# Kernel tuning notes

Hardware: AMD Instinct MI355X
Metric: run time of the kernel (lower is better)

The kernel has to match this reference:

```python
import jax, jax.numpy as jnp
import numpy as np

N_HEADS = 32
N_KV_HEADS = 8
DIM = 4096
HEAD_DIM = DIM // N_HEADS  # 128
N_REP = N_HEADS // N_KV_HEADS  # 4
MAX_B = 4
CACHE_LEN = 1024
SEQ = 1024
BATCH = 4


def _rope(t, cos, sin):
    # t: (b, s, h, hd); interpret last dim as interleaved complex pairs
    tr = t[..., 0::2]
    ti = t[..., 1::2]
    cos = cos[None, :, None, :]
    sin = sin[None, :, None, :]
    out_r = tr * cos - ti * sin
    out_i = tr * sin + ti * cos
    return jnp.stack([out_r, out_i], axis=-1).reshape(t.shape)


def setup_inputs() -> dict:
    key = jax.random.key(0)
    ks = jax.random.split(key, 6)
    x = jax.random.normal(ks[0], (BATCH, SEQ, DIM), dtype=jnp.float32)
    wq = jax.random.normal(ks[1], (DIM, N_HEADS * HEAD_DIM), dtype=jnp.float32) * (DIM ** -0.5)
    wk = jax.random.normal(ks[2], (DIM, N_KV_HEADS * HEAD_DIM), dtype=jnp.float32) * (DIM ** -0.5)
    wv = jax.random.normal(ks[3], (DIM, N_KV_HEADS * HEAD_DIM), dtype=jnp.float32) * (DIM ** -0.5)
    wo = jax.random.normal(ks[4], (DIM, DIM), dtype=jnp.float32) * (DIM ** -0.5)
    # standard RoPE frequencies, theta = 10000
    inv_freq = 1.0 / (10000.0 ** (np.arange(0, HEAD_DIM, 2, dtype=np.float32) / HEAD_DIM))
    pos = np.arange(SEQ, dtype=np.float32)
    ang = np.outer(pos, inv_freq)  # (SEQ, HEAD_DIM/2)
    freqs_cos = jnp.asarray(np.cos(ang), dtype=jnp.float32)
    freqs_sin = jnp.asarray(np.sin(ang), dtype=jnp.float32)
    return {"x": x, "freqs_cos": freqs_cos, "freqs_sin": freqs_sin,
            "wq": wq, "wk": wk, "wv": wv, "wo": wo, "start": 0}


def reference(x, freqs_cos, freqs_sin, wq, wk, wv, wo, start):
    b, s, _ = x.shape
    xq = (x @ wq).reshape(b, s, N_HEADS, HEAD_DIM)
    xk = (x @ wk).reshape(b, s, N_KV_HEADS, HEAD_DIM)
    xv = (x @ wv).reshape(b, s, N_KV_HEADS, HEAD_DIM)

    xq = _rope(xq, freqs_cos, freqs_sin)
    xk = _rope(xk, freqs_cos, freqs_sin)

    # KV cache append (cache initialized to zeros as in the module)
    cache_k = jnp.zeros((MAX_B, CACHE_LEN, N_KV_HEADS, HEAD_DIM), dtype=x.dtype)
    cache_v = jnp.zeros((MAX_B, CACHE_LEN, N_KV_HEADS, HEAD_DIM), dtype=x.dtype)
    cache_k = cache_k.at[:b, start:start + s].set(xk)
    cache_v = cache_v.at[:b, start:start + s].set(xv)

    keys = cache_k[:b, :start + s]    # (b, kv, n_kv, hd)
    values = cache_v[:b, :start + s]

    # repeat_kv to match query heads (GQA)
    keys = jnp.repeat(keys, N_REP, axis=2)      # (b, kv, n_q, hd)
    values = jnp.repeat(values, N_REP, axis=2)

    scale = 1.0 / jnp.sqrt(jnp.float32(HEAD_DIM)).astype(x.dtype)
    scores = jnp.einsum('bqhd,bkhd->bhqk', xq, keys) * scale
    probs = jax.nn.softmax(scores, axis=-1)
    out = jnp.einsum('bhqk,bkhd->bqhd', probs, values).reshape(b, s, DIM)
    return out @ wo
```

## Files before the change

kernel.cpp:

```cpp
#include <hip/hip_runtime.h>
#include <cstdint>

#define B_SZ 4
#define S_LEN 1024
#define DIM 4096
#define NH 32
#define KVH 8
#define HD 128
#define DQKV 6144

typedef __bf16 bf16x8 __attribute__((ext_vector_type(8)));
typedef float f32x4 __attribute__((ext_vector_type(4)));

__device__ __forceinline__ unsigned short f2bf(float f) {
  union { float f; uint32_t u; } v; v.f = f;
  uint32_t u = v.u;
  return (unsigned short)((u + 0x7fffu + ((u >> 16) & 1u)) >> 16);
}
__device__ __forceinline__ float bf2f(unsigned short h) {
  union { uint32_t u; float f; } v; v.u = ((uint32_t)h) << 16;
  return v.f;
}
__device__ __forceinline__ float ex2(float x) {
#if __has_builtin(__builtin_amdgcn_exp2f)
  return __builtin_amdgcn_exp2f(x);
#else
  return exp2f(x);
#endif
}

__device__ __forceinline__ void async16(void* lds, const void* g) {
  __builtin_amdgcn_global_load_lds(
      (const __attribute__((address_space(1))) void*)g,
      (__attribute__((address_space(3))) void*)lds, 16, 0, 0);
}

__global__ void cvt_x_kernel(const float* __restrict__ x, unsigned short* __restrict__ xb) {
  size_t i = ((size_t)blockIdx.x * 256 + threadIdx.x) * 4;
  float4 v = *(const float4*)(x + i);
  ushort4 o;
  o.x = f2bf(v.x); o.y = f2bf(v.y); o.z = f2bf(v.z); o.w = f2bf(v.w);
  *(ushort4*)(xb + i) = o;
}

__global__ void wtrans_kernel(const float* __restrict__ w, unsigned short* __restrict__ wt, int N) {
  __shared__ float tile[64][65];
  int n0 = blockIdx.x * 64, k0 = blockIdx.y * 64;
  int tx = threadIdx.x & 63, ty = threadIdx.x >> 6;
#pragma unroll
  for (int i = 0; i < 16; i++) {
    int k = ty + i * 4;
    tile[k][tx] = w[(size_t)(k0 + k) * N + n0 + tx];
  }
  __syncthreads();
  int c = threadIdx.x & 31, ny = threadIdx.x >> 5;
#pragma unroll
  for (int i = 0; i < 8; i++) {
    int n = ny + i * 8;
    ushort2 o;
    o.x = f2bf(tile[2 * c][n]);
    o.y = f2bf(tile[2 * c + 1][n]);
    *(ushort2*)(wt + (size_t)(n0 + n) * DIM + k0 + 2 * c) = o;
  }
}

template <bool OUT_BF16>
__global__ __launch_bounds__(512, 2) void gemm256_kernel(
    const unsigned short* __restrict__ A, const unsigned short* __restrict__ Bt,
    void* __restrict__ Cout, int Kdim, int ldc) {
  __shared__ __align__(16) unsigned short sh[3 * 16384];
  const int tid = threadIdx.x;
  const int wave = tid >> 6, lane = tid & 63;
  const int nbx = gridDim.x;
  const int nb = nbx * (int)gridDim.y;
  const int bid = (int)blockIdx.y * nbx + (int)blockIdx.x;
  const int sb = (bid & 7) * (nb >> 3) + (bid >> 3);
  const int m0 = (sb / nbx) * 256, n0 = (sb % nbx) * 256;

  const int r0 = tid >> 2;
  const int cs = (tid & 3) ^ ((r0 >> 1) & 3);
  const unsigned short* gA = A + (size_t)(m0 + r0) * Kdim + cs * 8;
  const unsigned short* gB = Bt + (size_t)(n0 + r0) * Kdim + cs * 8;
  const size_t halfstep = (size_t)128 * Kdim;

  const int wm = wave >> 2, wn = wave & 3;
  const int rl = lane & 15, lh4 = lane >> 4;
  const int pcl = lh4 ^ ((rl >> 1) & 3);
  const int aoff = (wm * 128 + rl) * 32 + pcl * 8;
  const int boff = (wn * 64 + rl) * 32 + pcl * 8;

  f32x4 acc[8][4] = {};

#define STAGE(CB, KO) do {                                        \
    unsigned short* dst = sh + (CB) * 16384 + wave * 512;         \
    async16(dst,          gA + (KO));                             \
    async16(dst + 4096,   gA + halfstep + (KO));                  \
    async16(dst + 8192,   gB + (KO));                             \
    async16(dst + 12288,  gB + halfstep + (KO));                  \
  } while (0)

#define COMPUTE(CB) do {                                                          \
    const unsigned short* bufA = sh + (CB) * 16384;                               \
    const unsigned short* bufB = bufA + 8192;                                     \
    bf16x8 bfr[4], afr[4];                                                        \
    _Pragma("unroll") for (int n = 0; n < 4; n++)                                 \
      bfr[n] = *(const bf16x8*)(bufB + boff + n * 512);                           \
    _Pragma("unroll") for (int m = 0; m < 4; m++)                                 \
      afr[m] = *(const bf16x8*)(bufA + aoff + m * 512);                           \
    __builtin_amdgcn_s_setprio(1);                                                \
    _Pragma("unroll") for (int m = 0; m < 4; m++)                                 \
      _Pragma("unroll") for (int n = 0; n < 4; n++)                               \
        acc[m][n] = __builtin_amdgcn_mfma_f32_16x16x32_bf16(afr[m], bfr[n], acc[m][n], 0, 0, 0); \
    __builtin_amdgcn_s_setprio(0);                                                \
    asm volatile("s_barrier" ::: "memory");                                       \
    _Pragma("unroll") for (int m = 0; m < 4; m++)                                 \
      afr[m] = *(const bf16x8*)(bufA + aoff + (m + 4) * 512);                     \
    __builtin_amdgcn_s_setprio(1);                                                \
    _Pragma("unroll") for (int m = 0; m < 4; m++)                                 \
      _Pragma("unroll") for (int n = 0; n < 4; n++)                               \
        acc[m + 4][n] = __builtin_amdgcn_mfma_f32_16x16x32_bf16(afr[m], bfr[n], acc[m + 4][n], 0, 0, 0); \
    __builtin_amdgcn_s_setprio(0);                                                \
  } while (0)

  STAGE(0, 0);
  STAGE(1, 32);
  STAGE(2, 64);
  const int NT = Kdim >> 5;
  int cb = 0;
  for (int t = 0; t < NT - 3; ++t) {
    asm volatile("s_waitcnt vmcnt(8)" ::: "memory");
    asm volatile("s_barrier" ::: "memory");
    COMPUTE(cb);
    asm volatile("s_waitcnt lgkmcnt(0)" ::: "memory");
    asm volatile("s_barrier" ::: "memory");
    STAGE(cb, (size_t)(t + 3) * 32);
    cb = cb == 2 ? 0 : cb + 1;
  }
  asm volatile("s_waitcnt vmcnt(8)" ::: "memory");
  asm volatile("s_barrier" ::: "memory");
  COMPUTE(cb);
  cb = cb == 2 ? 0 : cb + 1;
  asm volatile("s_waitcnt vmcnt(4)" ::: "memory");
  asm volatile("s_barrier" ::: "memory");
  COMPUTE(cb);
  cb = cb == 2 ? 0 : cb + 1;
  asm volatile("s_waitcnt vmcnt(0)" ::: "memory");
  asm volatile("s_barrier" ::: "memory");
  COMPUTE(cb);
#undef STAGE
#undef COMPUTE

#pragma unroll
  for (int m = 0; m < 8; m++)
#pragma unroll
    for (int n = 0; n < 4; n++)
#pragma unroll
      for (int reg = 0; reg < 4; reg++) {
        int row = m0 + wm * 128 + m * 16 + lh4 * 4 + reg;
        int col = n0 + wn * 64 + n * 16 + rl;
        float v = acc[m][n][reg];
        if (OUT_BF16)
          ((unsigned short*)Cout)[(size_t)row * ldc + col] = f2bf(v);
        else
          ((float*)Cout)[(size_t)row * ldc + col] = v;
      }
}

__global__ void rope_kernel(const unsigned short* __restrict__ src, const float* __restrict__ fc,
                            const float* __restrict__ fs, unsigned short* __restrict__ dst,
                            int nheads, int hshift, float scale) {
  int idx = blockIdx.x * 256 + threadIdx.x;
  int f4 = idx & 15;
  int rest = idx >> 4;
  int hh = rest & (nheads - 1);
  int t = rest >> hshift;
  int s = t & (S_LEN - 1);
  int b = t >> 10;
  union { uint4 v; unsigned short u[8]; } in, out;
  in.v = *(const uint4*)(src + (size_t)t * DQKV + hh * HD + f4 * 8);
  union { float4 v; float f[4]; } c4, s4;
  c4.v = *(const float4*)(fc + s * 64 + f4 * 4);
  s4.v = *(const float4*)(fs + s * 64 + f4 * 4);
#pragma unroll
  for (int j = 0; j < 4; j++) {
    float xr = bf2f(in.u[2 * j]), xi = bf2f(in.u[2 * j + 1]);
    float cc = c4.f[j], ss = s4.f[j];
    out.u[2 * j] = f2bf((xr * cc - xi * ss) * scale);
    out.u[2 * j + 1] = f2bf((xr * ss + xi * cc) * scale);
  }
  *(uint4*)(dst + ((size_t)(b * nheads + hh) * S_LEN + s) * HD + f4 * 8) = out.v;
}

__global__ void vtrans_kernel(const unsigned short* __restrict__ src, unsigned short* __restrict__ Vt) {
  __shared__ __align__(16) unsigned short tile[32][33];
  int s0 = blockIdx.x * 32, d0 = blockIdx.y * 32, bk = blockIdx.z;
  int tx = threadIdx.x & 31, ty = threadIdx.x >> 5;
#pragma unroll
  for (int i = 0; i < 4; i++) {
    int s = ty + i * 8;
    tile[s][tx] = src[(size_t)((bk >> 3) * S_LEN + s0 + s) * DQKV + (bk & 7) * HD + d0 + tx];
  }
  __syncthreads();
#pragma unroll
  for (int i = 0; i < 4; i++) {
    int d = ty + i * 8;
    Vt[((size_t)bk * HD + d0 + d) * S_LEN + s0 + tx] = tile[tx][d];
  }
}

__global__ __launch_bounds__(256, 3) void attn_kernel(
    const unsigned short* __restrict__ Qb,
    const unsigned short* __restrict__ Kb,
    const unsigned short* __restrict__ Vt,
    unsigned short* __restrict__ Ob) {
  __shared__ __align__(16) unsigned short Kt[64][128];
  __shared__ __align__(16) unsigned short Vl[128][64];
  __shared__ __align__(16) unsigned short Pl[4][16][72];
  const int tid = threadIdx.x, wave = tid >> 6, lane = tid & 63;
  const int qb = blockIdx.x, h = blockIdx.y, b = blockIdx.z;
  const int kvh = h >> 2;
  const int lql = lane & 15, lqh = lane >> 4;
  const int qrow = qb * 64 + wave * 16;

  const unsigned short* Qp = Qb + ((size_t)(b * NH + h) * S_LEN + qrow + lql) * HD + lqh * 8;
  bf16x8 qf[4];
#pragma unroll
  for (int kd = 0; kd < 4; kd++) qf[kd] = *(const bf16x8*)(Qp + kd * 32);

  const unsigned short* Kp = Kb + (size_t)(b * KVH + kvh) * S_LEN * HD;
  const unsigned short* Vp = Vt + (size_t)(b * KVH + kvh) * HD * S_LEN;
  const int krow_in = lane >> 4;
  const int kcol_sw = lane & 15;
  const int vrow_in = lane >> 3;
  const int vcol_off = ((lane & 7) ^ (lane >> 3)) * 8;

  float m_run[4], l_run[4];
  f32x4 Oacc[8] = {};
#pragma unroll
  for (int r = 0; r < 4; r++) { m_run[r] = -3.0e38f; l_run[r] = 0.0f; }

  for (int kt = 0; kt < S_LEN; kt += 64) {
    __syncthreads();
#pragma unroll
    for (int j = 0; j < 4; j++) {
      int rbase = wave * 16 + j * 4;
      int r = rbase + krow_in;
      async16(&Kt[rbase][0], Kp + (size_t)(kt + r) * HD + ((kcol_sw ^ (r & 7)) * 8));
    }
#pragma unroll
    for (int j = 0; j < 4; j++) {
      int dbase = wave * 32 + j * 8;
      int d = dbase + vrow_in;
      async16(&Vl[dbase][0], Vp + (size_t)d * S_LEN + kt + vcol_off);
    }
    __syncthreads();
    f32x4 sf[4] = {};
#pragma unroll
    for (int ni = 0; ni < 4; ni++) {
      const int ksw = lql & 7;
#pragma unroll
      for (int kd = 0; kd < 4; kd++) {
        bf16x8 kf = *(const bf16x8*)(&Kt[ni * 16 + lql][((kd * 4 + lqh) ^ ksw) * 8]);
        sf[ni] = __builtin_amdgcn_mfma_f32_16x16x32_bf16(qf[kd], kf, sf[ni], 0, 0, 0);
      }
    }
    float mnew[4], alpha[4], psum[4];
#pragma unroll
    for (int r = 0; r < 4; r++) {
      float v = fmaxf(fmaxf(sf[0][r], sf[1][r]), fmaxf(sf[2][r], sf[3][r]));
      v = fmaxf(v, __shfl_xor(v, 1));
      v = fmaxf(v, __shfl_xor(v, 2));
      v = fmaxf(v, __shfl_xor(v, 4));
      v = fmaxf(v, __shfl_xor(v, 8));
      mnew[r] = fmaxf(m_run[r], v);
      alpha[r] = ex2(m_run[r] - mnew[r]);
      m_run[r] = mnew[r];
      psum[r] = 0.0f;
    }
#pragma unroll
    for (int ni = 0; ni < 4; ni++)
#pragma unroll
      for (int r = 0; r < 4; r++) {
        float p = ex2(sf[ni][r] - mnew[r]);
        psum[r] += p;
        union { float f; uint32_t u; } pv; pv.f = p;
        Pl[wave][lqh * 4 + r][ni * 16 + lql] = (unsigned short)(pv.u >> 16);
      }
#pragma unroll
    for (int r = 0; r < 4; r++) {
      float v = psum[r];
      v += __shfl_xor(v, 1);
      v += __shfl_xor(v, 2);
      v += __shfl_xor(v, 4);
      v += __shfl_xor(v, 8);
      l_run[r] = l_run[r] * alpha[r] + v;
    }
#pragma unroll
    for (int ni = 0; ni < 8; ni++)
#pragma unroll
      for (int r = 0; r < 4; r++) Oacc[ni][r] *= alpha[r];
    bf16x8 pa[2];
#pragma unroll
    for (int ks = 0; ks < 2; ks++)
      pa[ks] = *(const bf16x8*)(&Pl[wave][lql][ks * 32 + lqh * 8]);
#pragma unroll
    for (int ni = 0; ni < 8; ni++) {
      const int ksw = lql & 7;
#pragma unroll
      for (int ks = 0; ks < 2; ks++) {
        bf16x8 vb = *(const bf16x8*)(&Vl[ni * 16 + lql][((ks * 4 + lqh) ^ ksw) * 8]);
        Oacc[ni] = __builtin_amdgcn_mfma_f32_16x16x32_bf16(pa[ks], vb, Oacc[ni], 0, 0, 0);
      }
    }
  }
#pragma unroll
  for (int r = 0; r < 4; r++) l_run[r] = 1.0f / l_run[r];
#pragma unroll
  for (int ni = 0; ni < 8; ni++)
#pragma unroll
    for (int r = 0; r < 4; r++) {
      int q = qrow + lqh * 4 + r;
      Ob[(size_t)(b * S_LEN + q) * DIM + h * HD + ni * 16 + lql] = f2bf(Oacc[ni][r] * l_run[r]);
    }
}

extern "C" void kernel_launch(void* const* d_in, const int* in_sizes, int n_in,
                              void* d_out, int out_size, void* d_ws, size_t ws_size,
                              hipStream_t stream) {
  (void)in_sizes; (void)n_in; (void)out_size; (void)ws_size;
  const float* x  = (const float*)d_in[0];
  const float* fc = (const float*)d_in[1];
  const float* fs = (const float*)d_in[2];
  const float* wq = (const float*)d_in[3];
  const float* wk = (const float*)d_in[4];
  const float* wv = (const float*)d_in[5];
  const float* wo = (const float*)d_in[6];
  float* out = (float*)d_out;
  char* ws = (char*)d_ws;

  const size_t MB = 1024 * 1024;
  unsigned short* xb    = (unsigned short*)(ws + 0);
  unsigned short* attnb = (unsigned short*)(ws + 0);
  unsigned short* wqkvt = (unsigned short*)(ws + 32 * MB);
  unsigned short* Qb    = (unsigned short*)(ws + 32 * MB);
  unsigned short* Kb    = (unsigned short*)(ws + 64 * MB);
  unsigned short* Vt    = (unsigned short*)(ws + 72 * MB);
  unsigned short* wot   = (unsigned short*)(ws + 80 * MB);
  unsigned short* qkv   = (unsigned short*)(ws + 112 * MB);

  cvt_x_kernel<<<16384, 256, 0, stream>>>(x, xb);
  wtrans_kernel<<<dim3(64, 64), 256, 0, stream>>>(wq, wqkvt, 4096);
  wtrans_kernel<<<dim3(16, 64), 256, 0, stream>>>(wk, wqkvt + (size_t)4096 * 4096, 1024);
  wtrans_kernel<<<dim3(16, 64), 256, 0, stream>>>(wv, wqkvt + (size_t)5120 * 4096, 1024);
  wtrans_kernel<<<dim3(64, 64), 256, 0, stream>>>(wo, wot, 4096);
  gemm256_kernel<true><<<dim3(DQKV / 256, 16), 512, 0, stream>>>(xb, wqkvt, qkv, DIM, DQKV);
  rope_kernel<<<8192, 256, 0, stream>>>(qkv, fc, fs, Qb, NH, 5, 0.12751879505099168f);
  rope_kernel<<<2048, 256, 0, stream>>>(qkv + 4096, fc, fs, Kb, KVH, 3, 1.0f);
  vtrans_kernel<<<dim3(32, 4, 32), 256, 0, stream>>>(qkv + 5120, Vt);
  attn_kernel<<<dim3(16, NH, B_SZ), 256, 0, stream>>>(Qb, Kb, Vt, attnb);
  gemm256_kernel<false><<<dim3(16, 16), 512, 0, stream>>>(attnb, wot, out, DIM, DIM);
}
```

Measured before the change: 785.2 us.

## Restructure GEMM mainloop to BK=64 double buffer with interleaved per-phase loads

Replaces the triple-buffered BK=32 pipeline with a double-buffered BK=64 scheme. The new XOR swizzle is over 8 chunks. Each K-tile is split into four phases, and each phase issues the async global-to-LDS loads for the next tile's A halves or the B halves two tiles ahead, interleaved with MFMA work. This is meant to halve barrier count per K and overlap memory with compute more finely. LDS use rises from 96KB to 128KB, which may hurt the 2-blocks-per-CU occupancy target. It also adds tricky waitcnt bookkeeping.

```diff
diff --git a/kernel.cpp b/kernel.cpp
--- a/kernel.cpp
+++ b/kernel.cpp
@@ -68,7 +68,7 @@
 __global__ __launch_bounds__(512, 2) void gemm256_kernel(
     const unsigned short* __restrict__ A, const unsigned short* __restrict__ Bt,
     void* __restrict__ Cout, int Kdim, int ldc) {
-  __shared__ __align__(16) unsigned short sh[3 * 16384];
+  __shared__ __align__(16) unsigned short sh[2 * 32768];
   const int tid = threadIdx.x;
   const int wave = tid >> 6, lane = tid & 63;
   const int nbx = gridDim.x;
@@ -77,78 +77,78 @@
   const int sb = (bid & 7) * (nb >> 3) + (bid >> 3);
   const int m0 = (sb / nbx) * 256, n0 = (sb % nbx) * 256;
 
-  const int r0 = tid >> 2;
-  const int cs = (tid & 3) ^ ((r0 >> 1) & 3);
-  const unsigned short* gA = A + (size_t)(m0 + r0) * Kdim + cs * 8;
-  const unsigned short* gB = Bt + (size_t)(n0 + r0) * Kdim + cs * 8;
-  const size_t halfstep = (size_t)128 * Kdim;
+  const int r0 = tid >> 3;
+  const int cs0 = (tid & 7) ^ (r0 & 7);
+  const unsigned short* gA = A + (size_t)(m0 + r0) * Kdim + cs0 * 8;
+  const unsigned short* gB = Bt + (size_t)(n0 + r0) * Kdim + cs0 * 8;
+  const size_t row64 = (size_t)64 * Kdim;
+  const size_t row128 = (size_t)128 * Kdim;
 
   const int wm = wave >> 2, wn = wave & 3;
   const int rl = lane & 15, lh4 = lane >> 4;
-  const int pcl = lh4 ^ ((rl >> 1) & 3);
-  const int aoff = (wm * 128 + rl) * 32 + pcl * 8;
-  const int boff = (wn * 64 + rl) * 32 + pcl * 8;
+  const int pc0 = (lh4 ^ (rl & 7)) * 8;
+  const int pc1 = ((lh4 + 4) ^ (rl & 7)) * 8;
+  const int arow = (wm * 128 + rl) * 64;
+  const int brow = (wn * 64 + rl) * 64;
 
   f32x4 acc[8][4] = {};
 
-#define STAGE(CB, KO) do {                                        \
-    unsigned short* dst = sh + (CB) * 16384 + wave * 512;         \
-    async16(dst,          gA + (KO));                             \
-    async16(dst + 4096,   gA + halfstep + (KO));                  \
-    async16(dst + 8192,   gB + (KO));                             \
-    async16(dst + 12288,  gB + halfstep + (KO));                  \
+#define STAGEH(BUF, AB, H, GS) do {                                               \
+    unsigned short* d_ = sh + (BUF) * 32768 + (AB) * 16384 + (H) * 8192 + wave * 512; \
+    async16(d_, (GS));                                                            \
+    async16(d_ + 4096, (GS) + row64);                                             \
   } while (0)
 
-#define COMPUTE(CB) do {                                                          \
-    const unsigned short* bufA = sh + (CB) * 16384;                               \
-    const unsigned short* bufB = bufA + 8192;                                     \
-    bf16x8 bfr[4], afr[4];                                                        \
-    _Pragma("unroll") for (int n = 0; n < 4; n++)                                 \
-      bfr[n] = *(const bf16x8*)(bufB + boff + n * 512);                           \
-    _Pragma("unroll") for (int m = 0; m < 4; m++)                                 \
-      afr[m] = *(const bf16x8*)(bufA + aoff + m * 512);                           \
+#define PHASEQ(Q, STAGE_STMT, WAIT_STMT) do {                                     \
+    af[0][0] = *(const bf16x8*)(bufA + arow + (2 * (Q)) * 1024 + pc0);            \
+    af[0][1] = *(const bf16x8*)(bufA + arow + (2 * (Q)) * 1024 + pc1);            \
+    af[1][0] = *(const bf16x8*)(bufA + arow + (2 * (Q) + 1) * 1024 + pc0);        \
+    af[1][1] = *(const bf16x8*)(bufA + arow + (2 * (Q) + 1) * 1024 + pc1);        \
+    STAGE_STMT;                                                                   \
+    WAIT_STMT;                                                                    \
+    __builtin_amdgcn_s_barrier();                                                 \
     __builtin_amdgcn_s_setprio(1);                                                \
-    _Pragma("unroll") for (int m = 0; m < 4; m++)                                 \
-      _Pragma("unroll") for (int n = 0; n < 4; n++)                               \
-        acc[m][n] = __builtin_amdgcn_mfma_f32_16x16x32_bf16(afr[m], bfr[n], acc[m][n], 0, 0, 0); \
+    _Pragma("unroll") for (int i = 0; i < 2; i++)                                 \
+      _Pragma("unroll") for (int n = 0; n < 4; n++) {                             \
+        acc[2 * (Q) + i][n] = __builtin_amdgcn_mfma_f32_16x16x32_bf16(            \
+            af[i][0], bf[n][0], acc[2 * (Q) + i][n], 0, 0, 0);                    \
+        acc[2 * (Q) + i][n] = __builtin_amdgcn_mfma_f32_16x16x32_bf16(            \
+            af[i][1], bf[n][1], acc[2 * (Q) + i][n], 0, 0, 0);                    \
+      }                                                                           \
     __builtin_amdgcn_s_setprio(0);                                                \
-    asm volatile("s_barrier" ::: "memory");                                       \
-    _Pragma("unroll") for (int m = 0; m < 4; m++)                                 \
-      afr[m] = *(const bf16x8*)(bufA + aoff + (m + 4) * 512);                     \
-    __builtin_amdgcn_s_setprio(1);                                                \
-    _Pragma("unroll") for (int m = 0; m < 4; m++)                                 \
-      _Pragma("unroll") for (int n = 0; n < 4; n++)                               \
-        acc[m + 4][n] = __builtin_amdgcn_mfma_f32_16x16x32_bf16(afr[m], bfr[n], acc[m + 4][n], 0, 0, 0); \
-    __builtin_amdgcn_s_setprio(0);                                                \
+    __builtin_amdgcn_s_barrier();                                                 \
   } while (0)
 
-  STAGE(0, 0);
-  STAGE(1, 32);
-  STAGE(2, 64);
-  const int NT = Kdim >> 5;
-  int cb = 0;
-  for (int t = 0; t < NT - 3; ++t) {
-    asm volatile("s_waitcnt vmcnt(8)" ::: "memory");
-    asm volatile("s_barrier" ::: "memory");
-    COMPUTE(cb);
-    asm volatile("s_waitcnt lgkmcnt(0)" ::: "memory");
-    asm volatile("s_barrier" ::: "memory");
-    STAGE(cb, (size_t)(t + 3) * 32);
-    cb = cb == 2 ? 0 : cb + 1;
-  }
-  asm volatile("s_waitcnt vmcnt(8)" ::: "memory");
-  asm volatile("s_barrier" ::: "memory");
-  COMPUTE(cb);
-  cb = cb == 2 ? 0 : cb + 1;
+  const int NT = Kdim >> 6;
+  STAGEH(0, 0, 0, gA);
+  STAGEH(0, 0, 1, gA + row128);
+  STAGEH(0, 1, 0, gB);
+  STAGEH(0, 1, 1, gB + row128);
+  STAGEH(1, 1, 0, gB + 64);
+  STAGEH(1, 1, 1, gB + row128 + 64);
   asm volatile("s_waitcnt vmcnt(4)" ::: "memory");
-  asm volatile("s_barrier" ::: "memory");
-  COMPUTE(cb);
-  cb = cb == 2 ? 0 : cb + 1;
-  asm volatile("s_waitcnt vmcnt(0)" ::: "memory");
-  asm volatile("s_barrier" ::: "memory");
-  COMPUTE(cb);
-#undef STAGE
-#undef COMPUTE
+  __builtin_amdgcn_s_barrier();
+
+  for (int t = 0; t < NT; ++t) {
+    const int cur = t & 1;
+    const unsigned short* bufA = sh + cur * 32768;
+    const unsigned short* bufB = bufA + 16384;
+    bf16x8 bf[4][2];
+    bf16x8 af[2][2];
+#pragma unroll
+    for (int n = 0; n < 4; n++) {
+      bf[n][0] = *(const bf16x8*)(bufB + brow + n * 1024 + pc0);
+      bf[n][1] = *(const bf16x8*)(bufB + brow + n * 1024 + pc1);
+    }
+    PHASEQ(0, if (t + 1 < NT) STAGEH(cur ^ 1, 0, 0, gA + (size_t)(t + 1) * 64), );
+    PHASEQ(1, if (t + 1 < NT) STAGEH(cur ^ 1, 0, 1, gA + row128 + (size_t)(t + 1) * 64), );
+    PHASEQ(2, if (t + 2 < NT) STAGEH(cur, 1, 0, gB + (size_t)(t + 2) * 64), );
+    PHASEQ(3, if (t + 2 < NT) STAGEH(cur, 1, 1, gB + row128 + (size_t)(t + 2) * 64),
+           if (t < NT - 2) { asm volatile("s_waitcnt vmcnt(4)" ::: "memory"); }
+           else if (t == NT - 2) { asm volatile("s_waitcnt vmcnt(0)" ::: "memory"); });
+  }
+#undef STAGEH
+#undef PHASEQ
 
 #pragma unroll
   for (int m = 0; m < 8; m++)
```

New measurement: 760.3 us. 1.03x faster.
